# Performance work log

Hardware: AMD Instinct MI355X
Metric: run time of the kernel (lower is better)

## Reference

```python
import jax, jax.numpy as jnp
import numpy as np

DIM = 512
HEADS = 8
WS = 8  # window_size


def setup_inputs() -> dict:
    key = jax.random.key(0)
    ks = jax.random.split(key, 7)
    b, c, h, w = 4, DIM, 192, 192
    x = jax.random.normal(ks[0], (b, c, h, w), dtype=jnp.float32)
    # conv1x1 weights are [out, in] matrices (kernel dim squeezed)
    wq = jax.random.normal(ks[1], (DIM, DIM), dtype=jnp.float32) * 0.02
    wk = jax.random.normal(ks[2], (DIM, DIM), dtype=jnp.float32) * 0.02
    wv = jax.random.normal(ks[3], (DIM, DIM), dtype=jnp.float32) * 0.02
    wo = jax.random.normal(ks[4], (DIM, DIM), dtype=jnp.float32) * 0.02
    bo = jax.random.normal(ks[5], (DIM,), dtype=jnp.float32) * 0.02
    # learned per-head additive bias over window tokens (trunc_normal std=0.02)
    beta = jax.random.normal(ks[6], (HEADS, WS * WS, WS * WS), dtype=jnp.float32) * 0.02
    return {"x": x, "wq": wq, "wk": wk, "wv": wv, "wo": wo, "bo": bo, "beta": beta}


def reference(x, wq, wk, wv, wo, bo, beta):
    b, c, h, w = x.shape
    s = WS
    pad_r = (-w) % s
    pad_b = (-h) % s
    x = jnp.pad(x, ((0, 0), (0, 0), (0, pad_b), (0, pad_r)))
    H, W = h + pad_b, w + pad_r
    nh, nw = H // s, W // s
    n = s * s
    head_dim = c // HEADS
    scale = head_dim ** -0.5
    # window partition: (b, c, nh, s, nw, s) -> (b*nh*nw, c, n)
    xw = x.reshape(b, c, nh, s, nw, s).transpose(0, 2, 4, 1, 3, 5).reshape(b * nh * nw, c, n)
    B = xw.shape[0]
    q = jnp.einsum('oc,bcn->bon', wq, xw).reshape(B, HEADS, head_dim, n)
    k = jnp.einsum('oc,bcn->bon', wk, xw).reshape(B, HEADS, head_dim, n)
    v = jnp.einsum('oc,bcn->bon', wv, xw).reshape(B, HEADS, head_dim, n)
    attn = jnp.einsum('bhdn,bhdm->bhnm', q, k) * scale + beta  # [B,H,n,n]
    attn = jax.nn.softmax(attn, axis=-1)
    o = jnp.einsum('bhnm,bhdm->bhdn', attn, v).reshape(B, c, n)
    o = jnp.einsum('oc,bcn->bon', wo, o) + bo[None, :, None]
    # window merge back to image
    out = o.reshape(b, nh, nw, c, s, s).transpose(0, 3, 1, 4, 2, 5).reshape(b, c, H, W)
    return out[:, :, :h, :w]
```

## Files before the change

kernel.cpp:

```cpp
#include <hip/hip_runtime.h>

typedef unsigned short ushort_t;
typedef __attribute__((ext_vector_type(4))) float f32x4;
typedef __attribute__((ext_vector_type(8))) short short8;

__device__ __forceinline__ ushort_t f2bf(float f) {
  union { float f; unsigned u; } v; v.f = f;
  unsigned r = v.u + 0x7fffu + ((v.u >> 16) & 1u);
  return (ushort_t)(r >> 16);
}

__global__ __launch_bounds__(256) void cvt_w_k(const float* __restrict__ wq,
                                               const float* __restrict__ wk,
                                               const float* __restrict__ wv,
                                               const float* __restrict__ wo,
                                               ushort_t* __restrict__ dst) {
  int idx = (blockIdx.x * 256 + threadIdx.x) * 4;
  int m = idx >> 18;
  int off = idx & 0x3ffff;
  const float* s = (m == 0) ? wq : (m == 1) ? wk : (m == 2) ? wv : wo;
  float4 v = *(const float4*)(s + off);
  ushort4 o;
  o.x = f2bf(v.x); o.y = f2bf(v.y); o.z = f2bf(v.z); o.w = f2bf(v.w);
  *(ushort4*)(dst + idx) = o;
}

__global__ __launch_bounds__(256) void xpose_k(const float* __restrict__ x,
                                               ushort_t* __restrict__ xT) {
  __shared__ ushort_t tile[128 * 80];
  int bid = blockIdx.x;
  int win = bid >> 2, kc = bid & 3;
  int b = win / 576, rem = win % 576, wh = rem / 24, ww = rem % 24;
  int tid = threadIdx.x;
  {
    int c_l = tid >> 1, half = tid & 1;
    const float* xb = x + (((b * 512 + kc * 128 + c_l) * 192 + wh * 8) * 192 + ww * 8);
#pragma unroll
    for (int ii = 0; ii < 4; ++ii) {
      int i = half * 4 + ii;
      float4 v0 = *(const float4*)(xb + i * 192);
      float4 v1 = *(const float4*)(xb + i * 192 + 4);
      uint4 u;
      u.x = (unsigned)f2bf(v0.x) | ((unsigned)f2bf(v0.y) << 16);
      u.y = (unsigned)f2bf(v0.z) | ((unsigned)f2bf(v0.w) << 16);
      u.z = (unsigned)f2bf(v1.x) | ((unsigned)f2bf(v1.y) << 16);
      u.w = (unsigned)f2bf(v1.z) | ((unsigned)f2bf(v1.w) << 16);
      *(uint4*)&tile[c_l * 80 + i * 8] = u;
    }
  }
  __syncthreads();
  {
    int tok = tid >> 2, q = tid & 3;
    unsigned w[16];
#pragma unroll
    for (int k = 0; k < 16; ++k) {
      unsigned lo = tile[(q * 32 + 2 * k) * 80 + tok];
      unsigned hi = tile[(q * 32 + 2 * k + 1) * 80 + tok];
      w[k] = lo | (hi << 16);
    }
    ushort_t* d = xT + ((win * 64 + tok) * 512 + kc * 128 + q * 32);
#pragma unroll
    for (int s2 = 0; s2 < 4; ++s2) {
      uint4 u; u.x = w[s2 * 4 + 0]; u.y = w[s2 * 4 + 1]; u.z = w[s2 * 4 + 2]; u.w = w[s2 * 4 + 3];
      *(uint4*)(d + s2 * 8) = u;
    }
  }
}

__global__ __launch_bounds__(512) void qkv_attn_k(const ushort_t* __restrict__ xT,
                                                  const ushort_t* __restrict__ wB,
                                                  const float* __restrict__ beta,
                                                  ushort_t* __restrict__ Og) {
  __shared__ ushort_t xws[64 * 520];
  __shared__ ushort_t qs[2][64 * 72];
  __shared__ ushort_t ks[2][64 * 72];
  __shared__ ushort_t vs[2][64 * 72];
  int win = blockIdx.x;
  int t0 = win * 64;
  int tid = threadIdx.x, lane = tid & 63, wid = tid >> 6;
  int l15 = lane & 15, l4 = lane >> 4;

  {
    int token = tid >> 3, cb = (tid & 7) * 64;
    const uint4* src = (const uint4*)(xT + (size_t)(t0 + token) * 512 + cb);
    uint4* dst = (uint4*)&xws[token * 520 + cb];
#pragma unroll
    for (int s2 = 0; s2 < 8; ++s2) dst[s2] = src[s2];
  }
  __syncthreads();

  const f32x4 z = {0.f, 0.f, 0.f, 0.f};

  for (int hcc = 0; hcc < 4; ++hcc) {
    f32x4 aq[4], ak[4], av[4];
#pragma unroll
    for (int i = 0; i < 4; ++i) { aq[i] = z; ak[i] = z; av[i] = z; }
    int ocol = hcc * 128 + wid * 16 + l15;
    const ushort_t* wqr = wB + (size_t)ocol * 512;
    const ushort_t* wkr = wB + 262144 + (size_t)ocol * 512;
    const ushort_t* wvr = wB + 524288 + (size_t)ocol * 512;
#pragma unroll
    for (int kk = 0; kk < 16; ++kk) {
      int cg = kk * 32 + l4 * 8;
      short8 bq = *(const short8*)(wqr + cg);
      short8 bk = *(const short8*)(wkr + cg);
      short8 bv = *(const short8*)(wvr + cg);
#pragma unroll
      for (int nt = 0; nt < 4; ++nt) {
        short8 a = *(const short8*)&xws[(nt * 16 + l15) * 520 + cg];
        aq[nt] = __builtin_amdgcn_mfma_f32_16x16x32_bf16(a, bq, aq[nt], 0, 0, 0);
        ak[nt] = __builtin_amdgcn_mfma_f32_16x16x32_bf16(a, bk, ak[nt], 0, 0, 0);
        av[nt] = __builtin_amdgcn_mfma_f32_16x16x32_bf16(a, bv, av[nt], 0, 0, 0);
      }
    }
    int hw = wid >> 2;
    int dd = (wid * 16 + l15) & 63;
#pragma unroll
    for (int nt = 0; nt < 4; ++nt) {
#pragma unroll
      for (int r = 0; r < 4; ++r) {
        int n = nt * 16 + l4 * 4 + r;
        qs[hw][n * 72 + dd] = f2bf(aq[nt][r]);
        ks[hw][n * 72 + dd] = f2bf(ak[nt][r]);
      }
      uint2 u;
      u.x = (unsigned)f2bf(av[nt][0]) | ((unsigned)f2bf(av[nt][1]) << 16);
      u.y = (unsigned)f2bf(av[nt][2]) | ((unsigned)f2bf(av[nt][3]) << 16);
      *(uint2*)&vs[hw][dd * 72 + nt * 16 + l4 * 4] = u;
    }
    __syncthreads();

    int hh = wid >> 2, rowg = wid & 3;
    int h = hcc * 2 + hh;
    f32x4 sA[4];
#pragma unroll
    for (int i = 0; i < 4; ++i) sA[i] = z;
#pragma unroll
    for (int kk = 0; kk < 2; ++kk) {
      short8 aF = *(const short8*)&qs[hh][(rowg * 16 + l15) * 72 + kk * 32 + l4 * 8];
#pragma unroll
      for (int mt = 0; mt < 4; ++mt) {
        short8 bF = *(const short8*)&ks[hh][(mt * 16 + l15) * 72 + kk * 32 + l4 * 8];
        sA[mt] = __builtin_amdgcn_mfma_f32_16x16x32_bf16(aF, bF, sA[mt], 0, 0, 0);
      }
    }
    const float* betah = beta + h * 4096;
    float p[4][4];
    float rmax[4] = {-1e30f, -1e30f, -1e30f, -1e30f};
#pragma unroll
    for (int mt = 0; mt < 4; ++mt)
#pragma unroll
      for (int r = 0; r < 4; ++r) {
        int n = rowg * 16 + l4 * 4 + r;
        float val = sA[mt][r] * 0.125f + betah[n * 64 + mt * 16 + l15];
        p[mt][r] = val;
        rmax[r] = fmaxf(rmax[r], val);
      }
#pragma unroll
    for (int m = 1; m <= 8; m <<= 1)
#pragma unroll
      for (int r = 0; r < 4; ++r) rmax[r] = fmaxf(rmax[r], __shfl_xor(rmax[r], m, 64));
    float rsum[4] = {0.f, 0.f, 0.f, 0.f};
#pragma unroll
    for (int mt = 0; mt < 4; ++mt)
#pragma unroll
      for (int r = 0; r < 4; ++r) {
        p[mt][r] = __expf(p[mt][r] - rmax[r]);
        rsum[r] += p[mt][r];
      }
#pragma unroll
    for (int m = 1; m <= 8; m <<= 1)
#pragma unroll
      for (int r = 0; r < 4; ++r) rsum[r] += __shfl_xor(rsum[r], m, 64);
    float rinv[4];
#pragma unroll
    for (int r = 0; r < 4; ++r) rinv[r] = 1.f / rsum[r];
    __syncthreads();
#pragma unroll
    for (int mt = 0; mt < 4; ++mt)
#pragma unroll
      for (int r = 0; r < 4; ++r)
        qs[hh][(rowg * 16 + l4 * 4 + r) * 72 + mt * 16 + l15] = f2bf(p[mt][r] * rinv[r]);
    __syncthreads();

    f32x4 oA[4];
#pragma unroll
    for (int i = 0; i < 4; ++i) oA[i] = z;
#pragma unroll
    for (int kk = 0; kk < 2; ++kk) {
      short8 aF = *(const short8*)&qs[hh][(rowg * 16 + l15) * 72 + kk * 32 + l4 * 8];
#pragma unroll
      for (int dt = 0; dt < 4; ++dt) {
        short8 bF = *(const short8*)&vs[hh][(dt * 16 + l15) * 72 + kk * 32 + l4 * 8];
        oA[dt] = __builtin_amdgcn_mfma_f32_16x16x32_bf16(aF, bF, oA[dt], 0, 0, 0);
      }
    }
#pragma unroll
    for (int dt = 0; dt < 4; ++dt)
#pragma unroll
      for (int r = 0; r < 4; ++r) {
        int n = rowg * 16 + l4 * 4 + r;
        Og[(size_t)(t0 + n) * 512 + h * 64 + dt * 16 + l15] = f2bf(oA[dt][r]);
      }
    __syncthreads();
  }
}

__global__ __launch_bounds__(256) void proj_k(const ushort_t* __restrict__ Og,
                                              const ushort_t* __restrict__ woB,
                                              const float* __restrict__ bo,
                                              float* __restrict__ out) {
  __shared__ ushort_t ows[64 * 136];
  int bid = blockIdx.x;
  int win = bid >> 1, mo = (bid & 1) * 256;
  int b = win / 576, rem = win % 576, wh = rem / 24, ww = rem % 24;
  int tid = threadIdx.x, lane = tid & 63, wid = tid >> 6;
  int l15 = lane & 15, l4 = lane >> 4;
  int t0 = win * 64;
  f32x4 z = {0.f, 0.f, 0.f, 0.f};
  f32x4 acc[4][4];
#pragma unroll
  for (int i = 0; i < 4; ++i)
#pragma unroll
    for (int j = 0; j < 4; ++j) acc[i][j] = z;
  int stok = tid >> 2, sq = tid & 3;
  for (int kcc = 0; kcc < 4; ++kcc) {
    {
      const uint4* src = (const uint4*)(Og + ((t0 + stok) * 512 + kcc * 128 + sq * 32));
      uint4* dstv = (uint4*)&ows[stok * 136 + sq * 32];
#pragma unroll
      for (int s2 = 0; s2 < 4; ++s2) dstv[s2] = src[s2];
    }
    __syncthreads();
#pragma unroll
    for (int kk = 0; kk < 4; ++kk) {
      short8 bF[4];
#pragma unroll
      for (int nt = 0; nt < 4; ++nt)
        bF[nt] = *(const short8*)&ows[(nt * 16 + l15) * 136 + kk * 32 + l4 * 8];
      int cg = kcc * 128 + kk * 32 + l4 * 8;
#pragma unroll
      for (int mt = 0; mt < 4; ++mt) {
        int orow = mo + wid * 64 + mt * 16 + l15;
        short8 aF = *(const short8*)(woB + orow * 512 + cg);
#pragma unroll
        for (int nt = 0; nt < 4; ++nt)
          acc[mt][nt] = __builtin_amdgcn_mfma_f32_16x16x32_bf16(aF, bF[nt], acc[mt][nt], 0, 0, 0);
      }
    }
    __syncthreads();
  }
#pragma unroll
  for (int mt = 0; mt < 4; ++mt) {
#pragma unroll
    for (int r = 0; r < 4; ++r) {
      int o = mo + wid * 64 + mt * 16 + l4 * 4 + r;
      float bias = bo[o];
#pragma unroll
      for (int nt = 0; nt < 4; ++nt) {
        int tok = nt * 16 + l15;
        int i = tok >> 3, j = tok & 7;
        out[((b * 512 + o) * 192 + wh * 8 + i) * 192 + ww * 8 + j] = acc[mt][nt][r] + bias;
      }
    }
  }
}

extern "C" void kernel_launch(void* const* d_in, const int* in_sizes, int n_in,
                              void* d_out, int out_size, void* d_ws, size_t ws_size,
                              hipStream_t stream) {
  const float* x    = (const float*)d_in[0];
  const float* wq   = (const float*)d_in[1];
  const float* wk   = (const float*)d_in[2];
  const float* wv   = (const float*)d_in[3];
  const float* wo   = (const float*)d_in[4];
  const float* bo   = (const float*)d_in[5];
  const float* beta = (const float*)d_in[6];

  ushort_t* wB = (ushort_t*)d_ws;
  ushort_t* Og = (ushort_t*)((char*)d_ws + (size_t)4 * 262144 * 2);
  ushort_t* xT = (ushort_t*)d_out;

  cvt_w_k<<<1024, 256, 0, stream>>>(wq, wk, wv, wo, wB);
  xpose_k<<<2304 * 4, 256, 0, stream>>>(x, xT);
  qkv_attn_k<<<2304, 512, 0, stream>>>(xT, wB, beta, Og);
  proj_k<<<2304 * 2, 256, 0, stream>>>(Og, wB + 3 * 262144, bo, (float*)d_out);
}
```

Baseline: 991.0 us.

## Fuse window transpose into attention kernel with swizzled LDS and remapped block order

Removes the separate transpose kernel: the attention kernel now reads fp32 x directly, converts it to bf16 and scatters it into a XOR-swizzled shared tile. This avoids the bf16 xT round trip through global memory. Block indices in both attention and projection are remapped across groups of 8, likely for XCD/L2 locality. Two __syncthreads around the softmax write-back into qs are dropped, which relies on each wave touching only its own row group. The new staging does scalar 2-byte LDS stores, which may cost more than the old vector copy.

Result: faster. 857.6 us (-13.5%).

```diff
diff --git a/kernel.cpp b/kernel.cpp
--- a/kernel.cpp
+++ b/kernel.cpp
@@ -8,6 +8,9 @@
   union { float f; unsigned u; } v; v.f = f;
   unsigned r = v.u + 0x7fffu + ((v.u >> 16) & 1u);
   return (ushort_t)(r >> 16);
+}
+__device__ __forceinline__ unsigned pack2(float lo, float hi) {
+  return (unsigned)f2bf(lo) | ((unsigned)f2bf(hi) << 16);
 }
 
 __global__ __launch_bounds__(256) void cvt_w_k(const float* __restrict__ wq,
@@ -25,89 +28,66 @@
   *(ushort4*)(dst + idx) = o;
 }
 
-__global__ __launch_bounds__(256) void xpose_k(const float* __restrict__ x,
-                                               ushort_t* __restrict__ xT) {
-  __shared__ ushort_t tile[128 * 80];
-  int bid = blockIdx.x;
-  int win = bid >> 2, kc = bid & 3;
-  int b = win / 576, rem = win % 576, wh = rem / 24, ww = rem % 24;
-  int tid = threadIdx.x;
-  {
-    int c_l = tid >> 1, half = tid & 1;
-    const float* xb = x + (((b * 512 + kc * 128 + c_l) * 192 + wh * 8) * 192 + ww * 8);
-#pragma unroll
-    for (int ii = 0; ii < 4; ++ii) {
-      int i = half * 4 + ii;
-      float4 v0 = *(const float4*)(xb + i * 192);
-      float4 v1 = *(const float4*)(xb + i * 192 + 4);
-      uint4 u;
-      u.x = (unsigned)f2bf(v0.x) | ((unsigned)f2bf(v0.y) << 16);
-      u.y = (unsigned)f2bf(v0.z) | ((unsigned)f2bf(v0.w) << 16);
-      u.z = (unsigned)f2bf(v1.x) | ((unsigned)f2bf(v1.y) << 16);
-      u.w = (unsigned)f2bf(v1.z) | ((unsigned)f2bf(v1.w) << 16);
-      *(uint4*)&tile[c_l * 80 + i * 8] = u;
-    }
-  }
-  __syncthreads();
-  {
-    int tok = tid >> 2, q = tid & 3;
-    unsigned w[16];
-#pragma unroll
-    for (int k = 0; k < 16; ++k) {
-      unsigned lo = tile[(q * 32 + 2 * k) * 80 + tok];
-      unsigned hi = tile[(q * 32 + 2 * k + 1) * 80 + tok];
-      w[k] = lo | (hi << 16);
-    }
-    ushort_t* d = xT + ((win * 64 + tok) * 512 + kc * 128 + q * 32);
-#pragma unroll
-    for (int s2 = 0; s2 < 4; ++s2) {
-      uint4 u; u.x = w[s2 * 4 + 0]; u.y = w[s2 * 4 + 1]; u.z = w[s2 * 4 + 2]; u.w = w[s2 * 4 + 3];
-      *(uint4*)(d + s2 * 8) = u;
-    }
-  }
-}
-
-__global__ __launch_bounds__(512) void qkv_attn_k(const ushort_t* __restrict__ xT,
-                                                  const ushort_t* __restrict__ wB,
-                                                  const float* __restrict__ beta,
-                                                  ushort_t* __restrict__ Og) {
+__global__ __launch_bounds__(512, 1) void qkv_attn4_k(const float* __restrict__ x,
+                                                      const ushort_t* __restrict__ wB,
+                                                      const float* __restrict__ beta,
+                                                      ushort_t* __restrict__ O) {
   __shared__ ushort_t xws[64 * 520];
   __shared__ ushort_t qs[2][64 * 72];
   __shared__ ushort_t ks[2][64 * 72];
   __shared__ ushort_t vs[2][64 * 72];
-  int win = blockIdx.x;
+  int bid = blockIdx.x;
+  int win = (bid & 7) * 288 + (bid >> 3);
+  int b = win / 576, rem = win % 576, wh = rem / 24, ww = rem % 24;
   int t0 = win * 64;
   int tid = threadIdx.x, lane = tid & 63, wid = tid >> 6;
   int l15 = lane & 15, l4 = lane >> 4;
 
-  {
-    int token = tid >> 3, cb = (tid & 7) * 64;
-    const uint4* src = (const uint4*)(xT + (size_t)(t0 + token) * 512 + cb);
-    uint4* dst = (uint4*)&xws[token * 520 + cb];
-#pragma unroll
-    for (int s2 = 0; s2 < 8; ++s2) dst[s2] = src[s2];
+#pragma unroll
+  for (int k = 0; k < 8; ++k) {
+    int u = tid + k * 512;
+    int c = u >> 3, i = u & 7;
+    const float* p = x + (((size_t)b * 512 + c) * 192 + wh * 8 + i) * 192 + ww * 8;
+    float4 v0 = *(const float4*)p;
+    float4 v1 = *(const float4*)(p + 4);
+    int colb = (((c >> 3) ^ i) << 3) + (c & 7);
+    ushort_t* dst = &xws[(i * 8) * 520 + colb];
+    dst[0 * 520] = f2bf(v0.x);
+    dst[1 * 520] = f2bf(v0.y);
+    dst[2 * 520] = f2bf(v0.z);
+    dst[3 * 520] = f2bf(v0.w);
+    dst[4 * 520] = f2bf(v1.x);
+    dst[5 * 520] = f2bf(v1.y);
+    dst[6 * 520] = f2bf(v1.z);
+    dst[7 * 520] = f2bf(v1.w);
   }
   __syncthreads();
 
   const f32x4 z = {0.f, 0.f, 0.f, 0.f};
+  int rowb[4], ii[4];
+#pragma unroll
+  for (int nt = 0; nt < 4; ++nt) {
+    rowb[nt] = (nt * 16 + l15) * 520;
+    ii[nt] = nt * 2 + (l15 >> 3);
+  }
 
   for (int hcc = 0; hcc < 4; ++hcc) {
     f32x4 aq[4], ak[4], av[4];
 #pragma unroll
     for (int i = 0; i < 4; ++i) { aq[i] = z; ak[i] = z; av[i] = z; }
     int ocol = hcc * 128 + wid * 16 + l15;
-    const ushort_t* wqr = wB + (size_t)ocol * 512;
-    const ushort_t* wkr = wB + 262144 + (size_t)ocol * 512;
-    const ushort_t* wvr = wB + 524288 + (size_t)ocol * 512;
+    const ushort_t* wqr = wB + (size_t)ocol * 512 + l4 * 8;
+    const ushort_t* wkr = wqr + 262144;
+    const ushort_t* wvr = wqr + 524288;
 #pragma unroll
     for (int kk = 0; kk < 16; ++kk) {
-      int cg = kk * 32 + l4 * 8;
-      short8 bq = *(const short8*)(wqr + cg);
-      short8 bk = *(const short8*)(wkr + cg);
-      short8 bv = *(const short8*)(wvr + cg);
+      short8 bq = *(const short8*)(wqr + kk * 32);
+      short8 bk = *(const short8*)(wkr + kk * 32);
+      short8 bv = *(const short8*)(wvr + kk * 32);
+      int cu = kk * 4 + l4;
 #pragma unroll
       for (int nt = 0; nt < 4; ++nt) {
-        short8 a = *(const short8*)&xws[(nt * 16 + l15) * 520 + cg];
+        short8 a = *(const short8*)&xws[rowb[nt] + ((cu ^ ii[nt]) << 3)];
         aq[nt] = __builtin_amdgcn_mfma_f32_16x16x32_bf16(a, bq, aq[nt], 0, 0, 0);
         ak[nt] = __builtin_amdgcn_mfma_f32_16x16x32_bf16(a, bk, ak[nt], 0, 0, 0);
         av[nt] = __builtin_amdgcn_mfma_f32_16x16x32_bf16(a, bv, av[nt], 0, 0, 0);
@@ -124,8 +104,8 @@
         ks[hw][n * 72 + dd] = f2bf(ak[nt][r]);
       }
       uint2 u;
-      u.x = (unsigned)f2bf(av[nt][0]) | ((unsigned)f2bf(av[nt][1]) << 16);
-      u.y = (unsigned)f2bf(av[nt][2]) | ((unsigned)f2bf(av[nt][3]) << 16);
+      u.x = pack2(av[nt][0], av[nt][1]);
+      u.y = pack2(av[nt][2], av[nt][3]);
       *(uint2*)&vs[hw][dd * 72 + nt * 16 + l4 * 4] = u;
     }
     __syncthreads();
@@ -175,13 +155,11 @@
     float rinv[4];
 #pragma unroll
     for (int r = 0; r < 4; ++r) rinv[r] = 1.f / rsum[r];
-    __syncthreads();
 #pragma unroll
     for (int mt = 0; mt < 4; ++mt)
 #pragma unroll
       for (int r = 0; r < 4; ++r)
         qs[hh][(rowg * 16 + l4 * 4 + r) * 72 + mt * 16 + l15] = f2bf(p[mt][r] * rinv[r]);
-    __syncthreads();
 
     f32x4 oA[4];
 #pragma unroll
@@ -200,19 +178,20 @@
 #pragma unroll
       for (int r = 0; r < 4; ++r) {
         int n = rowg * 16 + l4 * 4 + r;
-        Og[(size_t)(t0 + n) * 512 + h * 64 + dt * 16 + l15] = f2bf(oA[dt][r]);
-      }
-    __syncthreads();
-  }
-}
-
-__global__ __launch_bounds__(256) void proj_k(const ushort_t* __restrict__ Og,
-                                              const ushort_t* __restrict__ woB,
-                                              const float* __restrict__ bo,
-                                              float* __restrict__ out) {
+        O[(size_t)(t0 + n) * 512 + h * 64 + dt * 16 + l15] = f2bf(oA[dt][r]);
+      }
+    __syncthreads();
+  }
+}
+
+__global__ __launch_bounds__(256) void proj_kb(const ushort_t* __restrict__ O,
+                                               const ushort_t* __restrict__ woB,
+                                               const float* __restrict__ bo,
+                                               float* __restrict__ out) {
   __shared__ ushort_t ows[64 * 136];
   int bid = blockIdx.x;
-  int win = bid >> 1, mo = (bid & 1) * 256;
+  int wg = (bid & 7) * 576 + (bid >> 3);
+  int win = wg >> 1, mo = (wg & 1) * 256;
   int b = win / 576, rem = win % 576, wh = rem / 24, ww = rem % 24;
   int tid = threadIdx.x, lane = tid & 63, wid = tid >> 6;
   int l15 = lane & 15, l4 = lane >> 4;
@@ -226,7 +205,7 @@
   int stok = tid >> 2, sq = tid & 3;
   for (int kcc = 0; kcc < 4; ++kcc) {
     {
-      const uint4* src = (const uint4*)(Og + ((t0 + stok) * 512 + kcc * 128 + sq * 32));
+      const uint4* src = (const uint4*)(O + ((size_t)(t0 + stok) * 512 + kcc * 128 + sq * 32));
       uint4* dstv = (uint4*)&ows[stok * 136 + sq * 32];
 #pragma unroll
       for (int s2 = 0; s2 < 4; ++s2) dstv[s2] = src[s2];
@@ -242,7 +221,7 @@
 #pragma unroll
       for (int mt = 0; mt < 4; ++mt) {
         int orow = mo + wid * 64 + mt * 16 + l15;
-        short8 aF = *(const short8*)(woB + orow * 512 + cg);
+        short8 aF = *(const short8*)(woB + (size_t)orow * 512 + cg);
 #pragma unroll
         for (int nt = 0; nt < 4; ++nt)
           acc[mt][nt] = __builtin_amdgcn_mfma_f32_16x16x32_bf16(aF, bF[nt], acc[mt][nt], 0, 0, 0);
@@ -260,7 +239,7 @@
       for (int nt = 0; nt < 4; ++nt) {
         int tok = nt * 16 + l15;
         int i = tok >> 3, j = tok & 7;
-        out[((b * 512 + o) * 192 + wh * 8 + i) * 192 + ww * 8 + j] = acc[mt][nt][r] + bias;
+        out[(((size_t)b * 512 + o) * 192 + wh * 8 + i) * 192 + ww * 8 + j] = acc[mt][nt][r] + bias;
       }
     }
   }
@@ -278,11 +257,9 @@
   const float* beta = (const float*)d_in[6];
 
   ushort_t* wB = (ushort_t*)d_ws;
-  ushort_t* Og = (ushort_t*)((char*)d_ws + (size_t)4 * 262144 * 2);
-  ushort_t* xT = (ushort_t*)d_out;
+  ushort_t* O  = (ushort_t*)((char*)d_ws + (size_t)2097152);
 
   cvt_w_k<<<1024, 256, 0, stream>>>(wq, wk, wv, wo, wB);
-  xpose_k<<<2304 * 4, 256, 0, stream>>>(x, xT);
-  qkv_attn_k<<<2304, 512, 0, stream>>>(xT, wB, beta, Og);
-  proj_k<<<2304 * 2, 256, 0, stream>>>(Og, wB + 3 * 262144, bo, (float*)d_out);
-}
+  qkv_attn4_k<<<2304, 512, 0, stream>>>(x, wB, beta, O);
+  proj_kb<<<4608, 256, 0, stream>>>(O, wB + 3 * 262144, bo, (float*)d_out);
+}
```
